# Performance work log

Measured on AMD Instinct MI355X. Metric: run time of the kernel, lower is better.

Reference implementation:

```python
import jax, jax.numpy as jnp
import numpy as np

N = 2000      # batch_size * num_rois
PS = 7        # pool_size
C = 256       # roi-align channels
HID = 1024    # head width
NC = 81       # num_classes (COCO incl. background)
EPS = 1e-3    # keras BatchNormalization default epsilon


def setup_inputs() -> dict:
    key = jax.random.key(0)
    ks = jax.random.split(key, 6)
    sc = lambda k, shape, s: jax.random.normal(k, shape, jnp.float32) * s
    return {
        "pooled_rois": jax.random.normal(ks[0], (N, PS, PS, C), jnp.float32),
        # 7x7 VALID conv on a 7x7 input == flattened dense: [PS*PS*C, HID]
        "w1": sc(ks[1], (PS * PS * C, HID), 0.01),
        "b1": jnp.zeros((HID,), jnp.float32),
        "gamma1": jnp.ones((HID,), jnp.float32),
        "beta1": jnp.zeros((HID,), jnp.float32),
        # 1x1 conv == dense [HID, HID]
        "w2": sc(ks[2], (HID, HID), 0.02),
        "b2": jnp.zeros((HID,), jnp.float32),
        "gamma2": jnp.ones((HID,), jnp.float32),
        "beta2": jnp.zeros((HID,), jnp.float32),
        "w_logits": sc(ks[3], (HID, NC), 0.02),
        "b_logits": jnp.zeros((NC,), jnp.float32),
        "w_delta": sc(ks[4], (HID, NC * 4), 0.02),
        "b_delta": jnp.zeros((NC * 4,), jnp.float32),
    }


def _batchnorm_train(x, gamma, beta):
    # training=True: normalize with batch statistics over the RoI axis
    mu = jnp.mean(x, axis=0)
    var = jnp.var(x, axis=0)
    return gamma * (x - mu) * jax.lax.rsqrt(var + EPS) + beta


def reference(pooled_rois, w1, b1, gamma1, beta1, w2, b2, gamma2, beta2,
              w_logits, b_logits, w_delta, b_delta):
    n = pooled_rois.shape[0]
    # rcnn_class_conv1: 7x7 VALID conv on 7x7 input -> flatten + matmul
    x = pooled_rois.reshape(n, -1) @ w1 + b1          # [N, 1024]
    x = jax.nn.relu(_batchnorm_train(x, gamma1, beta1))
    # rcnn_class_conv2: 1x1 conv -> matmul
    x = x @ w2 + b2                                    # [N, 1024]
    x = jax.nn.relu(_batchnorm_train(x, gamma2, beta2))
    logits = x @ w_logits + b_logits                   # [N, NC]
    probs = jax.nn.softmax(logits, axis=-1)            # [N, NC]
    deltas = (x @ w_delta + b_delta).reshape(n, NC, 4) # [N, NC, 4]
    return logits, probs, deltas
```

## Files before the change

### kernel.cpp

```cpp
#include <hip/hip_runtime.h>

typedef unsigned short u16;
typedef __bf16 bf16x8 __attribute__((ext_vector_type(8)));
typedef float f32x4 __attribute__((ext_vector_type(4)));
typedef u16 u16x8 __attribute__((ext_vector_type(8)));

static constexpr int kNRoi = 2000;
static constexpr int kMPad = 2048;
static constexpr int kKin  = 12544;
static constexpr int kHid  = 1024;
static constexpr int kNOutPad = 512;
static constexpr int kNC = 81;
static constexpr int kND = 324;

__device__ __forceinline__ float bf2f(u16 h) {
  union { unsigned u; float f; } v; v.u = ((unsigned)h) << 16; return v.f;
}
__device__ __forceinline__ u16 f2bf(float f) {
  union { float f; unsigned u; } v; v.f = f;
  unsigned r = v.u + 0x7fffu + ((v.u >> 16) & 1u);
  return (u16)(r >> 16);
}

__global__ void sniff(const void* __restrict__ g, int* __restrict__ flag) {
  *flag = (((const unsigned*)g)[0] == 0x3f800000u) ? 1 : 0;
}

__global__ void to_bf16(const void* __restrict__ in, u16* __restrict__ out,
                        const int* __restrict__ flagp) {
  const int f32 = *flagp;
  long i = ((long)blockIdx.x * blockDim.x + threadIdx.x) * 8;
  u16x8 h;
  if (f32) {
    f32x4 a = *(const f32x4*)((const float*)in + i);
    f32x4 b = *(const f32x4*)((const float*)in + i + 4);
#pragma unroll
    for (int j = 0; j < 4; ++j) { h[j] = f2bf(a[j]); h[4 + j] = f2bf(b[j]); }
  } else {
    h = *(const u16x8*)((const u16*)in + i);
  }
  *(u16x8*)(out + i) = h;
}

__global__ void transpose_any(const void* __restrict__ in, u16* __restrict__ out,
                              int R, int C, const int* __restrict__ flagp) {
  __shared__ u16 t[32][33];
  const int f32 = *flagp;
  int tx = threadIdx.x & 31, ty = threadIdx.x >> 5;
  int cb = blockIdx.x * 32, rb = blockIdx.y * 32;
#pragma unroll
  for (int i = 0; i < 4; ++i) {
    int r = rb + ty + i * 8, c = cb + tx;
    if (r < R && c < C) {
      long idx = (long)r * C + c;
      t[ty + i * 8][tx] = f32 ? f2bf(((const float*)in)[idx]) : ((const u16*)in)[idx];
    }
  }
  __syncthreads();
#pragma unroll
  for (int i = 0; i < 4; ++i) {
    int c = cb + ty + i * 8, r = rb + tx;
    if (c < C && r < R) out[(long)c * R + r] = t[tx][ty + i * 8];
  }
}

__global__ __launch_bounds__(256) void gemm_bt(
    const u16* __restrict__ A, const u16* __restrict__ Bt,
    float* __restrict__ C, int Mreal, int K, int N, int kchunk) {
  __shared__ u16 As[128 * 32];
  __shared__ u16 Bs[128 * 32];
  const int tid  = threadIdx.x;
  const int lane = tid & 63;
  const int wave = tid >> 6;
  const int wm = (wave >> 1) * 64;
  const int wn = (wave & 1) * 64;

  f32x4 acc[4][4] = {};

  const int r0 = tid >> 2;
  const int kc = (tid & 3) * 8;
  long ar0 = (long)blockIdx.x * 128 + r0;      if (ar0 > Mreal - 1) ar0 = Mreal - 1;
  long ar1 = (long)blockIdx.x * 128 + 64 + r0; if (ar1 > Mreal - 1) ar1 = Mreal - 1;
  const long br0 = (long)blockIdx.y * 128 + r0;
  const long br1 = br0 + 64;

  const int kb = blockIdx.z * kchunk;
  const u16* ag0 = A + ar0 * K + kb + kc;
  const u16* ag1 = A + ar1 * K + kb + kc;
  const u16* bg0 = Bt + br0 * K + kb + kc;
  const u16* bg1 = Bt + br1 * K + kb + kc;

  u16* al0 = As + wave * 512;
  u16* al1 = As + 2048 + wave * 512;
  u16* bl0 = Bs + wave * 512;
  u16* bl1 = Bs + 2048 + wave * 512;

  const int fr = lane & 15;
  const int fq = (lane >> 4) * 8;

  const int iters = kchunk / 32;
  for (int it = 0; it < iters; ++it) {
    __builtin_amdgcn_global_load_lds((const __attribute__((address_space(1))) void*)ag0,
                                     (__attribute__((address_space(3))) void*)al0, 16, 0, 0);
    __builtin_amdgcn_global_load_lds((const __attribute__((address_space(1))) void*)ag1,
                                     (__attribute__((address_space(3))) void*)al1, 16, 0, 0);
    __builtin_amdgcn_global_load_lds((const __attribute__((address_space(1))) void*)bg0,
                                     (__attribute__((address_space(3))) void*)bl0, 16, 0, 0);
    __builtin_amdgcn_global_load_lds((const __attribute__((address_space(1))) void*)bg1,
                                     (__attribute__((address_space(3))) void*)bl1, 16, 0, 0);
    ag0 += 32; ag1 += 32; bg0 += 32; bg1 += 32;
    __syncthreads();

    bf16x8 afr[4], bfr[4];
#pragma unroll
    for (int i = 0; i < 4; ++i)
      afr[i] = *(const bf16x8*)(As + (wm + i * 16 + fr) * 32 + fq);
#pragma unroll
    for (int i = 0; i < 4; ++i)
      bfr[i] = *(const bf16x8*)(Bs + (wn + i * 16 + fr) * 32 + fq);
#pragma unroll
    for (int mi = 0; mi < 4; ++mi)
#pragma unroll
      for (int ni = 0; ni < 4; ++ni)
        acc[mi][ni] = __builtin_amdgcn_mfma_f32_16x16x32_bf16(afr[mi], bfr[ni], acc[mi][ni], 0, 0, 0);
    __syncthreads();
  }

  const int row0 = blockIdx.x * 128 + wm + (lane >> 4) * 4;
  const int col0 = blockIdx.y * 128 + wn + fr;
#pragma unroll
  for (int mi = 0; mi < 4; ++mi)
#pragma unroll
    for (int ni = 0; ni < 4; ++ni)
#pragma unroll
      for (int e = 0; e < 4; ++e)
        atomicAdd(&C[(long)(row0 + mi * 16 + e) * N + col0 + ni * 16], acc[mi][ni][e]);
}

__global__ void colstats(const float* __restrict__ X, float* __restrict__ S,
                         float* __restrict__ SS, int cols, int chunk) {
  int c = blockIdx.x * blockDim.x + threadIdx.x;
  int r0 = blockIdx.y * chunk;
  float s = 0.f, ss = 0.f;
  for (int r = r0; r < r0 + chunk; ++r) {
    float v = X[(long)r * cols + c];
    s += v; ss += v * v;
  }
  atomicAdd(&S[c], s);
  atomicAdd(&SS[c], ss);
}

__global__ void finalize_stats(const float* __restrict__ S, const float* __restrict__ SS,
                               const void* __restrict__ gamma, const void* __restrict__ beta,
                               float* __restrict__ SV, float* __restrict__ TV,
                               int n, float invN, const int* __restrict__ flagp) {
  const int f32 = *flagp;
  int c = blockIdx.x * blockDim.x + threadIdx.x;
  if (c < n) {
    float g = f32 ? ((const float*)gamma)[c] : bf2f(((const u16*)gamma)[c]);
    float b = f32 ? ((const float*)beta)[c]  : bf2f(((const u16*)beta)[c]);
    float mu = S[c] * invN;
    float var = SS[c] * invN - mu * mu;
    float sc = g * rsqrtf(var + 1e-3f);
    SV[c] = sc;
    TV[c] = b - mu * sc;
  }
}

__global__ void bn_relu_kernel(const float* __restrict__ X, const float* __restrict__ SV,
                               const float* __restrict__ TV, u16* __restrict__ H) {
  long i = ((long)blockIdx.x * blockDim.x + threadIdx.x) * 8;
  int c = (int)(i & (kHid - 1));
  f32x4 x0 = *(const f32x4*)(X + i);
  f32x4 x1 = *(const f32x4*)(X + i + 4);
  f32x4 s0 = *(const f32x4*)(SV + c);
  f32x4 s1 = *(const f32x4*)(SV + c + 4);
  f32x4 t0 = *(const f32x4*)(TV + c);
  f32x4 t1 = *(const f32x4*)(TV + c + 4);
  u16x8 h;
#pragma unroll
  for (int j = 0; j < 4; ++j) {
    h[j]     = f2bf(fmaxf(0.f, s0[j] * x0[j] + t0[j]));
    h[4 + j] = f2bf(fmaxf(0.f, s1[j] * x1[j] + t1[j]));
  }
  *(u16x8*)(H + i) = h;
}

__global__ void head_out(const float* __restrict__ X, const void* __restrict__ blv,
                         const void* __restrict__ bdv, void* __restrict__ outv,
                         const int* __restrict__ flagp) {
  const int f32 = *flagp;
  int lane = threadIdx.x & 63;
  int row = blockIdx.x * 4 + (threadIdx.x >> 6);
  if (row >= kNRoi) return;
  const float* xr = X + (long)row * kNOutPad;
  auto ldb = [&](const void* p, int i) -> float {
    return f32 ? ((const float*)p)[i] : bf2f(((const u16*)p)[i]);
  };
  auto st = [&](long i, float v) {
    if (f32) ((float*)outv)[i] = v; else ((u16*)outv)[i] = f2bf(v);
  };
  float v0 = xr[lane] + ldb(blv, lane);
  float v1 = (lane < kNC - 64) ? xr[64 + lane] + ldb(blv, 64 + lane) : -3.0e38f;
  float m = fmaxf(v0, v1);
#pragma unroll
  for (int off = 32; off > 0; off >>= 1) m = fmaxf(m, __shfl_xor(m, off, 64));
  float e0 = __expf(v0 - m);
  float e1 = (lane < kNC - 64) ? __expf(v1 - m) : 0.f;
  float s = e0 + e1;
#pragma unroll
  for (int off = 32; off > 0; off >>= 1) s += __shfl_xor(s, off, 64);
  float inv = 1.f / s;
  long lo = (long)row * kNC;
  long pr = (long)kNRoi * kNC + lo;
  long de = 2L * kNRoi * kNC + (long)row * kND;
  st(lo + lane, v0);
  st(pr + lane, e0 * inv);
  if (lane < kNC - 64) { st(lo + 64 + lane, v1); st(pr + 64 + lane, e1 * inv); }
#pragma unroll
  for (int j = 0; j < 5; ++j) {
    int c = lane + 64 * j;
    st(de + c, xr[kNC + c] + ldb(bdv, c));
  }
  if (lane < 4) { int c = lane + 320; st(de + c, xr[kNC + c] + ldb(bdv, c)); }
}

extern "C" void kernel_launch(void* const* d_in, const int* in_sizes, int n_in,
                              void* d_out, int out_size, void* d_ws, size_t ws_size,
                              hipStream_t stream) {
  const void* pooled   = d_in[0];
  const void* w1       = d_in[1];
  const void* gamma1   = d_in[3];
  const void* beta1    = d_in[4];
  const void* w2       = d_in[5];
  const void* gamma2   = d_in[7];
  const void* beta2    = d_in[8];
  const void* w_logits = d_in[9];
  const void* b_logits = d_in[10];
  const void* w_delta  = d_in[11];
  const void* b_delta  = d_in[12];

  char* ws = (char*)d_ws;
  u16*   W1T  = (u16*)(ws + 0);
  u16*   W2T  = (u16*)(ws + 25690112);
  u16*   WHT  = (u16*)(ws + 27787264);
  float* BUFA = (float*)(ws + 28835840);
  u16*   BUFB = (u16*)(ws + 37224448);
  float* S    = (float*)(ws + 41418752);
  float* SS   = S + 1024;
  float* SV   = S + 2048;
  float* TV   = S + 3072;
  int*   FLAG = (int*)(S + 4096);
  u16*   A1   = (u16*)(ws + 41451520);

  const float invN = 1.f / (float)kNRoi;

  sniff<<<1, 1, 0, stream>>>(gamma1, FLAG);

  to_bf16<<<12250, 256, 0, stream>>>(pooled, A1, FLAG);

  hipMemsetAsync(WHT, 0, (size_t)kNOutPad * kHid * sizeof(u16), stream);
  transpose_any<<<dim3(32, 392), 256, 0, stream>>>(w1, W1T, kKin, kHid, FLAG);
  transpose_any<<<dim3(32, 32),  256, 0, stream>>>(w2, W2T, kHid, kHid, FLAG);
  transpose_any<<<dim3(3, 32),   256, 0, stream>>>(w_logits, WHT, kHid, kNC, FLAG);
  transpose_any<<<dim3(11, 32),  256, 0, stream>>>(w_delta, WHT + (long)kNC * kHid, kHid, kND, FLAG);

  hipMemsetAsync(BUFA, 0, (size_t)kMPad * kHid * sizeof(float), stream);
  gemm_bt<<<dim3(16, 8, 8), 256, 0, stream>>>(A1, W1T, BUFA, kNRoi, kKin, kHid, kKin / 8);

  hipMemsetAsync(S, 0, 2 * kHid * sizeof(float), stream);
  colstats<<<dim3(kHid / 256, 40), 256, 0, stream>>>(BUFA, S, SS, kHid, kNRoi / 40);
  finalize_stats<<<kHid / 256, 256, 0, stream>>>(S, SS, gamma1, beta1, SV, TV, kHid, invN, FLAG);
  bn_relu_kernel<<<(kMPad * kHid) / (256 * 8), 256, 0, stream>>>(BUFA, SV, TV, BUFB);

  hipMemsetAsync(BUFA, 0, (size_t)kMPad * kHid * sizeof(float), stream);
  gemm_bt<<<dim3(16, 8, 2), 256, 0, stream>>>(BUFB, W2T, BUFA, kMPad, kHid, kHid, kHid / 2);

  hipMemsetAsync(S, 0, 2 * kHid * sizeof(float), stream);
  colstats<<<dim3(kHid / 256, 40), 256, 0, stream>>>(BUFA, S, SS, kHid, kNRoi / 40);
  finalize_stats<<<kHid / 256, 256, 0, stream>>>(S, SS, gamma2, beta2, SV, TV, kHid, invN, FLAG);
  bn_relu_kernel<<<(kMPad * kHid) / (256 * 8), 256, 0, stream>>>(BUFA, SV, TV, BUFB);

  hipMemsetAsync(BUFA, 0, (size_t)kMPad * kNOutPad * sizeof(float), stream);
  gemm_bt<<<dim3(16, 4, 4), 256, 0, stream>>>(BUFB, WHT, BUFA, kMPad, kHid, kNOutPad, kHid / 4);

  head_out<<<kNRoi / 4, 256, 0, stream>>>(BUFA, b_logits, b_delta, d_out, FLAG);
}
```

Baseline: 456.7 us.

## Double-buffer GEMM LDS tiles, vectorize weight transposes, widen colstats grid

The GEMM now ping-pongs between two LDS buffers, issuing the next tile's global-to-LDS loads right after the barrier so they overlap the MFMA work on the current tile. This also removes one barrier per iteration. The large weight transposes use a 64x64 tile with vectorized 4-wide loads and 8-wide stores instead of scalar 32x32 accesses. Column statistics run with twice as many row chunks to expose more parallelism. The risks are doubled LDS use, which may lower occupancy, and a possible race, since the single barrier has to cover both the reuse of the alternate buffer and the completion of the async loads.

After: 428.6 us. 6.1% less time.

```diff
diff --git a/kernel.cpp b/kernel.cpp
--- a/kernel.cpp
+++ b/kernel.cpp
@@ -4,6 +4,7 @@
 typedef __bf16 bf16x8 __attribute__((ext_vector_type(8)));
 typedef float f32x4 __attribute__((ext_vector_type(4)));
 typedef u16 u16x8 __attribute__((ext_vector_type(8)));
+typedef u16 u16x4 __attribute__((ext_vector_type(4)));
 
 static constexpr int kNRoi = 2000;
 static constexpr int kMPad = 2048;
@@ -42,6 +43,42 @@
   *(u16x8*)(out + i) = h;
 }
 
+__global__ void transpose_fast(const void* __restrict__ in, u16* __restrict__ out,
+                               int R, int C, const int* __restrict__ flagp) {
+  __shared__ u16 t[64 * 72];
+  const int f32 = *flagp;
+  const int tid = threadIdx.x;
+  const int cb = blockIdx.x * 64, rb = blockIdx.y * 64;
+  const int rl = tid >> 4;
+  const int cl = (tid & 15) * 4;
+#pragma unroll
+  for (int i = 0; i < 4; ++i) {
+    int r = rl + i * 16;
+    long idx = (long)(rb + r) * C + cb + cl;
+    u16 h[4];
+    if (f32) {
+      f32x4 v = *(const f32x4*)((const float*)in + idx);
+#pragma unroll
+      for (int j = 0; j < 4; ++j) h[j] = f2bf(v[j]);
+    } else {
+      u16x4 v = *(const u16x4*)((const u16*)in + idx);
+#pragma unroll
+      for (int j = 0; j < 4; ++j) h[j] = v[j];
+    }
+#pragma unroll
+    for (int j = 0; j < 4; ++j) t[(cl + j) * 72 + r] = h[j];
+  }
+  __syncthreads();
+  const int c2 = tid >> 3;
+  const int r2 = (tid & 7) * 8;
+#pragma unroll
+  for (int i = 0; i < 2; ++i) {
+    int c = c2 + i * 32;
+    u16x8 v = *(const u16x8*)&t[c * 72 + r2];
+    *(u16x8*)(out + (long)(cb + c) * R + rb + r2) = v;
+  }
+}
+
 __global__ void transpose_any(const void* __restrict__ in, u16* __restrict__ out,
                               int R, int C, const int* __restrict__ flagp) {
   __shared__ u16 t[32][33];
@@ -67,8 +104,8 @@
 __global__ __launch_bounds__(256) void gemm_bt(
     const u16* __restrict__ A, const u16* __restrict__ Bt,
     float* __restrict__ C, int Mreal, int K, int N, int kchunk) {
-  __shared__ u16 As[128 * 32];
-  __shared__ u16 Bs[128 * 32];
+  __shared__ u16 As[2][128 * 32];
+  __shared__ u16 Bs[2][128 * 32];
   const int tid  = threadIdx.x;
   const int lane = tid & 63;
   const int wave = tid >> 6;
@@ -90,41 +127,47 @@
   const u16* bg0 = Bt + br0 * K + kb + kc;
   const u16* bg1 = Bt + br1 * K + kb + kc;
 
-  u16* al0 = As + wave * 512;
-  u16* al1 = As + 2048 + wave * 512;
-  u16* bl0 = Bs + wave * 512;
-  u16* bl1 = Bs + 2048 + wave * 512;
-
   const int fr = lane & 15;
   const int fq = (lane >> 4) * 8;
-
   const int iters = kchunk / 32;
+
+#define STAGE(b) do {                                                          \
+    u16* al_ = As[b] + wave * 512;                                             \
+    u16* bl_ = Bs[b] + wave * 512;                                             \
+    __builtin_amdgcn_global_load_lds((const __attribute__((address_space(1))) void*)ag0, \
+                                     (__attribute__((address_space(3))) void*)al_, 16, 0, 0); \
+    __builtin_amdgcn_global_load_lds((const __attribute__((address_space(1))) void*)ag1, \
+                                     (__attribute__((address_space(3))) void*)(al_ + 2048), 16, 0, 0); \
+    __builtin_amdgcn_global_load_lds((const __attribute__((address_space(1))) void*)bg0, \
+                                     (__attribute__((address_space(3))) void*)bl_, 16, 0, 0); \
+    __builtin_amdgcn_global_load_lds((const __attribute__((address_space(1))) void*)bg1, \
+                                     (__attribute__((address_space(3))) void*)(bl_ + 2048), 16, 0, 0); \
+    ag0 += 32; ag1 += 32; bg0 += 32; bg1 += 32;                                \
+  } while (0)
+
+  STAGE(0);
+  int buf = 0;
   for (int it = 0; it < iters; ++it) {
-    __builtin_amdgcn_global_load_lds((const __attribute__((address_space(1))) void*)ag0,
-                                     (__attribute__((address_space(3))) void*)al0, 16, 0, 0);
-    __builtin_amdgcn_global_load_lds((const __attribute__((address_space(1))) void*)ag1,
-                                     (__attribute__((address_space(3))) void*)al1, 16, 0, 0);
-    __builtin_amdgcn_global_load_lds((const __attribute__((address_space(1))) void*)bg0,
-                                     (__attribute__((address_space(3))) void*)bl0, 16, 0, 0);
-    __builtin_amdgcn_global_load_lds((const __attribute__((address_space(1))) void*)bg1,
-                                     (__attribute__((address_space(3))) void*)bl1, 16, 0, 0);
-    ag0 += 32; ag1 += 32; bg0 += 32; bg1 += 32;
     __syncthreads();
-
+    if (it + 1 < iters) STAGE(buf ^ 1);
+
+    const u16* as_ = As[buf];
+    const u16* bs_ = Bs[buf];
     bf16x8 afr[4], bfr[4];
 #pragma unroll
     for (int i = 0; i < 4; ++i)
-      afr[i] = *(const bf16x8*)(As + (wm + i * 16 + fr) * 32 + fq);
+      afr[i] = *(const bf16x8*)(as_ + (wm + i * 16 + fr) * 32 + fq);
 #pragma unroll
     for (int i = 0; i < 4; ++i)
-      bfr[i] = *(const bf16x8*)(Bs + (wn + i * 16 + fr) * 32 + fq);
+      bfr[i] = *(const bf16x8*)(bs_ + (wn + i * 16 + fr) * 32 + fq);
 #pragma unroll
     for (int mi = 0; mi < 4; ++mi)
 #pragma unroll
       for (int ni = 0; ni < 4; ++ni)
         acc[mi][ni] = __builtin_amdgcn_mfma_f32_16x16x32_bf16(afr[mi], bfr[ni], acc[mi][ni], 0, 0, 0);
-    __syncthreads();
-  }
+    buf ^= 1;
+  }
+#undef STAGE
 
   const int row0 = blockIdx.x * 128 + wm + (lane >> 4) * 4;
   const int col0 = blockIdx.y * 128 + wn + fr;
@@ -260,8 +303,8 @@
   to_bf16<<<12250, 256, 0, stream>>>(pooled, A1, FLAG);
 
   hipMemsetAsync(WHT, 0, (size_t)kNOutPad * kHid * sizeof(u16), stream);
-  transpose_any<<<dim3(32, 392), 256, 0, stream>>>(w1, W1T, kKin, kHid, FLAG);
-  transpose_any<<<dim3(32, 32),  256, 0, stream>>>(w2, W2T, kHid, kHid, FLAG);
+  transpose_fast<<<dim3(16, 196), 256, 0, stream>>>(w1, W1T, kKin, kHid, FLAG);
+  transpose_fast<<<dim3(16, 16),  256, 0, stream>>>(w2, W2T, kHid, kHid, FLAG);
   transpose_any<<<dim3(3, 32),   256, 0, stream>>>(w_logits, WHT, kHid, kNC, FLAG);
   transpose_any<<<dim3(11, 32),  256, 0, stream>>>(w_delta, WHT + (long)kNC * kHid, kHid, kND, FLAG);
 
@@ -269,7 +312,7 @@
   gemm_bt<<<dim3(16, 8, 8), 256, 0, stream>>>(A1, W1T, BUFA, kNRoi, kKin, kHid, kKin / 8);
 
   hipMemsetAsync(S, 0, 2 * kHid * sizeof(float), stream);
-  colstats<<<dim3(kHid / 256, 40), 256, 0, stream>>>(BUFA, S, SS, kHid, kNRoi / 40);
+  colstats<<<dim3(kHid / 256, 80), 256, 0, stream>>>(BUFA, S, SS, kHid, kNRoi / 80);
   finalize_stats<<<kHid / 256, 256, 0, stream>>>(S, SS, gamma1, beta1, SV, TV, kHid, invN, FLAG);
   bn_relu_kernel<<<(kMPad * kHid) / (256 * 8), 256, 0, stream>>>(BUFA, SV, TV, BUFB);
 
@@ -277,7 +320,7 @@
   gemm_bt<<<dim3(16, 8, 2), 256, 0, stream>>>(BUFB, W2T, BUFA, kMPad, kHid, kHid, kHid / 2);
 
   hipMemsetAsync(S, 0, 2 * kHid * sizeof(float), stream);
-  colstats<<<dim3(kHid / 256, 40), 256, 0, stream>>>(BUFA, S, SS, kHid, kNRoi / 40);
+  colstats<<<dim3(kHid / 256, 80), 256, 0, stream>>>(BUFA, S, SS, kHid, kNRoi / 80);
   finalize_stats<<<kHid / 256, 256, 0, stream>>>(S, SS, gamma2, beta2, SV, TV, kHid, invN, FLAG);
   bn_relu_kernel<<<(kMPad * kHid) / (256 * 8), 256, 0, stream>>>(BUFA, SV, TV, BUFB);
 
```
